# Kernel tuning notes

Hardware: AMD Instinct MI355X
Metric: run time of the kernel (lower is better)

## Reference

```python
import jax, jax.numpy as jnp
import numpy as np
from jax import lax

N, M, T, IN, H, DEPTH = 64, 10, 160, 40, 256, 3
B = N * M
EPS = 1e-8


def setup_inputs() -> dict:
    key = jax.random.key(0)
    ks = jax.random.split(key, 20)
    s = 1.0 / np.sqrt(H)  # torch LSTM init scale
    inp = {
        "sequences": jax.random.normal(ks[0], (B, T, IN), jnp.float32),
        "len_sequences": jax.random.randint(ks[1], (B,), 80, T + 1, jnp.int32),
        "w_sim": jnp.float32(0.5),
        "b_sim": jnp.float32(0.5),
    }
    in_sizes = [IN, H, H]
    for l in range(DEPTH):
        k = 2 + 4 * l
        inp[f"Wih{l}"] = jax.random.uniform(ks[k], (4 * H, in_sizes[l]), jnp.float32, -s, s)
        inp[f"Whh{l}"] = jax.random.uniform(ks[k + 1], (4 * H, H), jnp.float32, -s, s)
        inp[f"bih{l}"] = jax.random.uniform(ks[k + 2], (4 * H,), jnp.float32, -s, s)
        inp[f"bhh{l}"] = jax.random.uniform(ks[k + 3], (4 * H,), jnp.float32, -s, s)
    return inp


def _lstm_layer(x_tbf, mask_tb, Wih, Whh, bih, bhh):
    """x_tbf: [T,B,F] time-major. mask_tb: [T,B] valid-step mask.
    Returns (h_seq [T,B,H], c_last [B,H]) where c_last is the cell state at
    the last valid timestep of each sequence (packed-sequence semantics)."""
    b = x_tbf.shape[1]
    h0 = jnp.zeros((b, H), x_tbf.dtype)
    c0 = jnp.zeros((b, H), x_tbf.dtype)

    def step(carry, xm):
        h, c = carry
        xt, mt = xm
        g = xt @ Wih.T + bih + h @ Whh.T + bhh  # [B,4H]
        i, f, gg, o = jnp.split(g, 4, axis=1)
        cn = jax.nn.sigmoid(f) * c + jax.nn.sigmoid(i) * jnp.tanh(gg)
        hn = jax.nn.sigmoid(o) * jnp.tanh(cn)
        m = mt[:, None]
        h2 = jnp.where(m, hn, h)
        c2 = jnp.where(m, cn, c)
        return (h2, c2), h2

    (hT, cT), h_seq = lax.scan(step, (h0, c0), (x_tbf, mask_tb))
    return h_seq, cT


def reference(sequences, len_sequences, Wih0, Whh0, bih0, bhh0,
              Wih1, Whh1, bih1, bhh1, Wih2, Whh2, bih2, bhh2,
              w_sim, b_sim):
    lens = len_sequences.astype(jnp.int32)
    x = jnp.transpose(sequences, (1, 0, 2))  # [T,B,IN]
    mask = jnp.arange(T)[:, None] < lens[None, :]  # [T,B]

    layers = [(Wih0, Whh0, bih0, bhh0), (Wih1, Whh1, bih1, bhh1), (Wih2, Whh2, bih2, bhh2)]
    c_last = None
    for (Wih, Whh, bih, bhh) in layers:
        x, c_last = _lstm_layer(x, mask, Wih, Whh, bih, bhh)
    E = c_last  # [B,H] final-layer cell state per utterance (original order)

    # L2-normalize embeddings (F.normalize, p=2, dim=1)
    E = E / jnp.maximum(jnp.linalg.norm(E, axis=1, keepdims=True), 1e-12)

    Er = E.reshape(N, M, H)
    C = Er.mean(axis=1)  # [N,H] speaker centroids
    # exclusive centroids exactly as source: (M*c_j + E_i)/(M-1)
    Cm = ((M * C[:, None, :] + Er) / (M - 1)).reshape(B, H)

    En = E / jnp.maximum(jnp.linalg.norm(E, axis=1, keepdims=True), EPS)
    Cn = C / jnp.maximum(jnp.linalg.norm(C, axis=1, keepdims=True), EPS)
    Cmn = Cm / jnp.maximum(jnp.linalg.norm(Cm, axis=1, keepdims=True), EPS)

    S = (En @ Cn.T) * w_sim + b_sim  # [B,N]: cos(E_i, c_j)*w + b

    # diagonal block: row i, col i//M uses exclusive centroid
    d = jnp.sum(En * Cmn, axis=1)  # [B]
    rows = jnp.arange(B)
    cols = jnp.repeat(jnp.arange(N), M)
    S = S.at[rows, cols].set(d * w_sim + b_sim)
    return S


if __name__ == "__main__":
    out = reference(**setup_inputs())
    print(out.shape, out.dtype)
```

## Files before the change

kernel.cpp:

```cpp
#include <hip/hip_runtime.h>
#include <cstdint>
#include <cstddef>

typedef __attribute__((ext_vector_type(8))) short short8;
typedef __attribute__((ext_vector_type(4))) float f32x4;
typedef __attribute__((ext_vector_type(4))) unsigned short us4;

#define N_SPK 64
#define M_UTT 10
#define T_SEQ 160
#define IN_F  40
#define H_DIM 256
#define B_TOT 640
#define G4    1024
#define FSTR  64

__device__ __forceinline__ unsigned short f2bf(float f) {
  unsigned int u = __float_as_uint(f);
  u += 0x7FFFu + ((u >> 16) & 1u);
  return (unsigned short)(u >> 16);
}
__device__ __forceinline__ float b2f(unsigned short u) {
  return __uint_as_float(((unsigned int)u) << 16);
}
__device__ __forceinline__ float sigm(float x) {
  return 1.f / (1.f + __expf(-x));
}
__device__ __forceinline__ float tanh_fast(float x) {
  return 1.f - 2.f / (1.f + __expf(2.f * x));
}
__device__ __forceinline__ unsigned long long ato_ld(const unsigned long long* p) {
  return __hip_atomic_load(p, __ATOMIC_RELAXED, __HIP_MEMORY_SCOPE_AGENT);
}
__device__ __forceinline__ void ato_st(unsigned long long* p, unsigned long long v) {
  __hip_atomic_store(p, v, __ATOMIC_RELAXED, __HIP_MEMORY_SCOPE_AGENT);
}
__device__ __forceinline__ int flg_ld(const int* p) {
  return __hip_atomic_load(p, __ATOMIC_RELAXED, __HIP_MEMORY_SCOPE_AGENT);
}
__device__ __forceinline__ void flg_st(int* p, int v) {
  __hip_atomic_store(p, v, __ATOMIC_RELAXED, __HIP_MEMORY_SCOPE_AGENT);
}

__global__ void pack_w_kernel(const float* __restrict__ W, short* __restrict__ out,
                              int Kin, int Ktiles) {
  int idx = blockIdx.x * 256 + threadIdx.x;
  int total = 64 * Ktiles * 64;
  if (idx >= total) return;
  int lane = idx & 63;
  int rest = idx >> 6;
  int ks   = rest % Ktiles;
  int tile = rest / Ktiles;
  int n  = tile * 16 + (lane & 15);
  int k0 = ks * 32 + (lane >> 4) * 8;
  short8 v;
#pragma unroll
  for (int j = 0; j < 8; ++j) {
    int k = k0 + j;
    float f = (k < Kin) ? W[(size_t)n * Kin + k] : 0.f;
    v[j] = (short)f2bf(f);
  }
  *(short8*)&out[(size_t)idx * 8] = v;
}

__global__ void bias_sum_kernel(const float* __restrict__ a, const float* __restrict__ b,
                                float* __restrict__ o) {
  int i = blockIdx.x * 256 + threadIdx.x;
  if (i < G4) o[i] = a[i] + b[i];
}

__global__ __launch_bounds__(256, 2)
void gate_gemm0(const float* __restrict__ seq, const short* __restrict__ Wp,
                const float* __restrict__ bias, unsigned short* __restrict__ G) {
  const int btile = blockIdx.x % 40;
  const int rest  = blockIdx.x / 40;
  const int tg    = rest & 3;
  const int chunk = rest >> 2;
  const int tid = threadIdx.x, lane = tid & 63, wave = tid >> 6;
  const int nl = lane & 15, mq = lane >> 4;

  for (int mg = 0; mg < 4; ++mg) {
    const int t0 = chunk * 16 + mg * 4;
    f32x4 acc[4][4];
#pragma unroll
    for (int q = 0; q < 4; ++q) {
      int tile = tg * 16 + wave + 4 * q;
      float bv = bias[tile * 16 + nl];
#pragma unroll
      for (int mm = 0; mm < 4; ++mm) acc[mm][q] = (f32x4){bv, bv, bv, bv};
    }
    for (int kt = 0; kt < 2; ++kt) {
      short8 a[4];
      const int m = btile * 16 + nl;
      const int k0 = kt * 32 + mq * 8;
#pragma unroll
      for (int mm = 0; mm < 4; ++mm) {
#pragma unroll
        for (int j = 0; j < 8; ++j) {
          int k = k0 + j;
          float f = (k < IN_F) ? seq[((size_t)m * T_SEQ + (t0 + mm)) * IN_F + k] : 0.f;
          a[mm][j] = (short)f2bf(f);
        }
      }
#pragma unroll
      for (int q = 0; q < 4; ++q) {
        int tile = tg * 16 + wave + 4 * q;
        short8 b = *(const short8*)&Wp[(((size_t)tile * 2 + kt) * 64 + lane) * 8];
#pragma unroll
        for (int mm = 0; mm < 4; ++mm)
          acc[mm][q] = __builtin_amdgcn_mfma_f32_16x16x32_bf16(a[mm], b, acc[mm][q], 0, 0, 0);
      }
    }
#pragma unroll
    for (int mm = 0; mm < 4; ++mm)
#pragma unroll
      for (int q = 0; q < 4; ++q) {
        int tile = tg * 16 + wave + 4 * q;
        us4 o;
#pragma unroll
        for (int r = 0; r < 4; ++r) o[r] = f2bf(acc[mm][q][r]);
        *(us4*)&G[(((size_t)(t0 + mm) * 40 + btile) * 64 + tile) * 256 + lane * 4] = o;
      }
  }
}

template<int L>
__device__ __forceinline__ void rec_stage(
    int S, int hb,
    const short* __restrict__ Whhp, const short* __restrict__ Wihp,
    const unsigned short* __restrict__ G0, const float* __restrict__ biasl,
    unsigned long long* __restrict__ hxch, int* __restrict__ flags,
    const int* __restrict__ lens, float* __restrict__ c_state,
    unsigned short* h_sh, unsigned short* x_sh,
    float* bias_sh, short* wih_lds, int* len_sh)
{
  const int tid = threadIdx.x, lane = tid & 63, wave = tid >> 6;
  const int mq = lane >> 4, nl = lane & 15;
  const int lc = wave * 16 + nl;
  const int colown = hb * 64 + lc;
  unsigned long long* x64 = (unsigned long long*)x_sh;

  short8 wregH[4][8];
#pragma unroll
  for (int g = 0; g < 4; ++g) {
    const int tile = g * 16 + hb * 4 + wave;
#pragma unroll
    for (int kt = 0; kt < 8; ++kt)
      wregH[g][kt] = *(const short8*)&Whhp[(((size_t)tile * 8 + kt) * 64 + lane) * 8];
  }
  short8 wregI[4][4];
  if (L >= 1) {
#pragma unroll
    for (int g = 0; g < 4; ++g) {
      const int tile = g * 16 + hb * 4 + wave;
#pragma unroll
      for (int kt = 0; kt < 4; ++kt)
        wregI[g][kt] = *(const short8*)&Wihp[(((size_t)tile * 8 + kt) * 64 + lane) * 8];
    }
    for (int i = tid; i < 4096; i += 256) {
      int tl = i >> 6, ln = i & 63;
      int lt = tl >> 2, kt4 = tl & 3;
      int gt = (lt >> 2) * 16 + hb * 4 + (lt & 3);
      *(short8*)&wih_lds[(lt * 4 + kt4) * 512 + ln * 8] =
          *(const short8*)&Wihp[(((size_t)gt * 8 + 4 + kt4) * 64 + ln) * 8];
    }
    for (int i = tid; i < 1024; i += 256) bias_sh[i] = biasl[i];
  }
  for (int i = tid; i < 64 * 264; i += 256) h_sh[i] = 0;
  if (tid < 64) len_sh[tid] = lens[S * 64 + tid];

  float creg[16];
#pragma unroll
  for (int i = 0; i < 16; ++i) creg[i] = 0.f;

  if (L == 0) {
    us4 tmp[16];
#pragma unroll
    for (int m = 0; m < 4; ++m)
#pragma unroll
      for (int g = 0; g < 4; ++g) {
        const int tile = g * 16 + hb * 4 + wave;
        tmp[m * 4 + g] = *(const us4*)&G0[(((size_t)0 * 40 + S * 4 + m) * 64 + tile) * 256 + lane * 4];
      }
#pragma unroll
    for (int u = 0; u < 16; ++u)
      x64[u * 256 + tid] = *(unsigned long long*)&tmp[u];
  }
  __syncthreads();

  const int fself = L * 40 + S * 4 + hb;

  unsigned long long xr[16];
  if (L >= 1) {
    if (tid < 4)
      while (flg_ld(&flags[((L - 1) * 40 + S * 4 + tid) * FSTR]) < 1) {}
    __syncthreads();
    const unsigned long long* xb0 =
        hxch + ((size_t)((0 * 3 + (L - 1)) * 10 + S)) * 4096;
#pragma unroll
    for (int u = 0; u < 16; ++u) xr[u] = ato_ld(&xb0[u * 256 + tid]);
  }

  for (int t = 0; t < T_SEQ; ++t) {
    const int par = t & 3;

    if (L < 2 && tid < 4)
      while (flg_ld(&flags[((L + 1) * 40 + S * 4 + tid) * FSTR]) < t - 3) {}

    if (L >= 1) {
#pragma unroll
      for (int u = 0; u < 16; ++u) {
        int j = u * 256 + tid, pp = j >> 10, jj = j & 1023;
        *(unsigned long long*)&x_sh[(jj >> 4) * 264 + pp * 64 + (jj & 15) * 4] = xr[u];
      }
      __syncthreads();
    }
    f32x4 acc[4][4];
    if (L == 0) {
#pragma unroll
      for (int m = 0; m < 4; ++m)
#pragma unroll
        for (int g = 0; g < 4; ++g) {
          unsigned long long v = x64[(m * 4 + g) * 256 + tid];
          us4 gv = *(us4*)&v;
#pragma unroll
          for (int r = 0; r < 4; ++r) acc[m][g][r] = b2f(gv[r]);
        }
    } else {
#pragma unroll
      for (int g = 0; g < 4; ++g) {
        const int tile = g * 16 + hb * 4 + wave;
        float bv = bias_sh[tile * 16 + nl];
#pragma unroll
        for (int m = 0; m < 4; ++m) acc[m][g] = (f32x4){bv, bv, bv, bv};
      }
    }
#pragma unroll
    for (int kt = 0; kt < 8; ++kt) {
      short8 a[4];
#pragma unroll
      for (int m = 0; m < 4; ++m)
        a[m] = *(const short8*)&h_sh[(m * 16 + nl) * 264 + kt * 32 + mq * 8];
#pragma unroll
      for (int m = 0; m < 4; ++m)
#pragma unroll
        for (int g = 0; g < 4; ++g)
          acc[m][g] = __builtin_amdgcn_mfma_f32_16x16x32_bf16(a[m], wregH[g][kt], acc[m][g], 0, 0, 0);
    }
    if (L >= 1) {
#pragma unroll
      for (int kt = 0; kt < 8; ++kt) {
        short8 a[4];
#pragma unroll
        for (int m = 0; m < 4; ++m)
          a[m] = *(const short8*)&x_sh[(m * 16 + nl) * 264 + kt * 32 + mq * 8];
#pragma unroll
        for (int g = 0; g < 4; ++g) {
          short8 b = (kt < 4) ? wregI[g][kt]
                              : *(const short8*)&wih_lds[((g * 4 + wave) * 4 + (kt - 4)) * 512 + lane * 8];
#pragma unroll
          for (int m = 0; m < 4; ++m)
            acc[m][g] = __builtin_amdgcn_mfma_f32_16x16x32_bf16(a[m], b, acc[m][g], 0, 0, 0);
        }
      }
    }
    unsigned short hv[16];
#pragma unroll
    for (int m = 0; m < 4; ++m)
#pragma unroll
      for (int r = 0; r < 4; ++r) {
        const int row = m * 16 + mq * 4 + r;
        float c_old = creg[m * 4 + r];
        float cn = sigm(acc[m][1][r]) * c_old + sigm(acc[m][0][r]) * tanh_fast(acc[m][2][r]);
        float hn = sigm(acc[m][3][r]) * tanh_fast(cn);
        bool upd = t < len_sh[row];
        if (upd) creg[m * 4 + r] = cn;
        hv[m * 4 + r] = upd ? f2bf(hn) : h_sh[row * 264 + colown];
      }
    __syncthreads();
#pragma unroll
    for (int m = 0; m < 4; ++m)
#pragma unroll
      for (int r = 0; r < 4; ++r)
        h_sh[(m * 16 + mq * 4 + r) * 264 + colown] = hv[m * 4 + r];
    __syncthreads();
    unsigned long long* myslab =
        hxch + ((size_t)((par * 3 + L) * 10 + S) * 4 + hb) * 1024;
    for (int j = tid; j < 1024; j += 256) {
      int sample = j >> 4, l4 = j & 15;
      unsigned long long v =
          *(const unsigned long long*)&h_sh[sample * 264 + hb * 64 + l4 * 4];
      ato_st(&myslab[j], v);
    }
    __syncthreads();
    if (tid == 0) flg_st(&flags[fself * FSTR], t + 1);
    if (L == 0) {
      int tn = (t + 1 < T_SEQ) ? t + 1 : t;
      us4 tmp[16];
#pragma unroll
      for (int m = 0; m < 4; ++m)
#pragma unroll
        for (int g = 0; g < 4; ++g) {
          const int tile = g * 16 + hb * 4 + wave;
          tmp[m * 4 + g] = *(const us4*)&G0[(((size_t)tn * 40 + S * 4 + m) * 64 + tile) * 256 + lane * 4];
        }
#pragma unroll
      for (int u = 0; u < 16; ++u)
        x64[u * 256 + tid] = *(unsigned long long*)&tmp[u];
    }
    if (t + 1 < T_SEQ) {
      if (tid < 3) {
        int p = tid + (tid >= hb ? 1 : 0);
        while (flg_ld(&flags[(L * 40 + S * 4 + p) * FSTR]) < t + 1) {}
      }
      if (L >= 1 && tid >= 64 && tid < 68)
        while (flg_ld(&flags[((L - 1) * 40 + S * 4 + (tid - 64)) * FSTR]) < t + 2) {}
      __syncthreads();
      if (L >= 1) {
        const unsigned long long* xb =
            hxch + ((size_t)((((t + 1) & 3) * 3 + (L - 1)) * 10 + S)) * 4096;
#pragma unroll
        for (int u = 0; u < 16; ++u) xr[u] = ato_ld(&xb[u * 256 + tid]);
      }
      {
        unsigned long long pr[12];
#pragma unroll
        for (int u = 0; u < 12; ++u) {
          int j = u * 256 + tid;
          int pp = j >> 10, jj = j & 1023;
          int p = pp + (pp >= hb ? 1 : 0);
          pr[u] = ato_ld(&hxch[((size_t)((par * 3 + L) * 10 + S) * 4 + p) * 1024 + jj]);
        }
#pragma unroll
        for (int u = 0; u < 12; ++u) {
          int j = u * 256 + tid;
          int pp = j >> 10, jj = j & 1023;
          int p = pp + (pp >= hb ? 1 : 0);
          *(unsigned long long*)&h_sh[(jj >> 4) * 264 + p * 64 + (jj & 15) * 4] = pr[u];
        }
      }
      __syncthreads();
    }
  }
  if (L == 2) {
#pragma unroll
    for (int m = 0; m < 4; ++m)
#pragma unroll
      for (int r = 0; r < 4; ++r) {
        const int row = m * 16 + mq * 4 + r;
        c_state[((size_t)S * 64 + row) * 256 + colown] = creg[m * 4 + r];
      }
  }
}

__global__ __launch_bounds__(256, 1)
void fused_lstm(const short* __restrict__ Whhp_all, const short* __restrict__ Wih1p,
                const short* __restrict__ Wih2p, const float* __restrict__ biasc,
                const unsigned short* __restrict__ G0, const int* __restrict__ lens,
                unsigned long long* __restrict__ hxch, int* __restrict__ flags,
                float* __restrict__ c_state)
{
  __shared__ unsigned short h_sh[64 * 264];
  __shared__ unsigned short x_sh[64 * 264];
  __shared__ float bias_sh[1024];
  __shared__ short wih_lds[16 * 4 * 512];
  __shared__ int len_sh[64];

  const int bid  = blockIdx.x;
  const int xcd  = bid & 7;
  const int j    = bid >> 3;
  const int g    = (j >> 2) * 8 + xcd;
  if (g >= 30) return;
  const int L  = g / 10;
  const int S  = g % 10;
  const int hb = j & 3;

  if (L == 0)
    rec_stage<0>(S, hb, Whhp_all,          nullptr, G0, nullptr,
                 hxch, flags, lens, c_state, h_sh, x_sh, bias_sh, wih_lds, len_sh);
  else if (L == 1)
    rec_stage<1>(S, hb, Whhp_all + 262144, Wih1p, G0, biasc + G4,
                 hxch, flags, lens, c_state, h_sh, x_sh, bias_sh, wih_lds, len_sh);
  else
    rec_stage<2>(S, hb, Whhp_all + 524288, Wih2p, G0, biasc + 2 * G4,
                 hxch, flags, lens, c_state, h_sh, x_sh, bias_sh, wih_lds, len_sh);
}

__global__ void k_norm(const float* __restrict__ E, float* __restrict__ E1,
                       float* __restrict__ En) {
  int row  = blockIdx.x * 4 + (threadIdx.x >> 6);
  int lane = threadIdx.x & 63;
  const float* e = E + (size_t)row * H_DIM;
  float v[4]; float ss = 0.f;
#pragma unroll
  for (int j = 0; j < 4; ++j) { v[j] = e[lane + 64 * j]; ss += v[j] * v[j]; }
#pragma unroll
  for (int m = 32; m >= 1; m >>= 1) ss += __shfl_xor(ss, m, 64);
  float nrm  = sqrtf(ss);
  float inv1 = 1.f / fmaxf(nrm, 1e-12f);
  float inv2 = 1.f / fmaxf(nrm * inv1, 1e-8f);
#pragma unroll
  for (int j = 0; j < 4; ++j) {
    float e1 = v[j] * inv1;
    E1[(size_t)row * H_DIM + lane + 64 * j] = e1;
    En[(size_t)row * H_DIM + lane + 64 * j] = e1 * inv2;
  }
}

__global__ void k_cent(const float* __restrict__ E1, float* __restrict__ C,
                       float* __restrict__ CnT) {
  int n = blockIdx.x;
  int lane = threadIdx.x;
  float v[4]; float ss = 0.f;
#pragma unroll
  for (int j = 0; j < 4; ++j) {
    int col = lane + 64 * j;
    float s = 0.f;
    for (int m = 0; m < M_UTT; ++m) s += E1[((size_t)n * M_UTT + m) * H_DIM + col];
    v[j] = s / (float)M_UTT;
    ss += v[j] * v[j];
  }
#pragma unroll
  for (int m = 32; m >= 1; m >>= 1) ss += __shfl_xor(ss, m, 64);
  float inv = 1.f / fmaxf(sqrtf(ss), 1e-8f);
#pragma unroll
  for (int j = 0; j < 4; ++j) {
    int col = lane + 64 * j;
    C[(size_t)n * H_DIM + col]  = v[j];
    CnT[(size_t)col * N_SPK + n] = v[j] * inv;
  }
}

__global__ void k_cm(const float* __restrict__ E1, const float* __restrict__ C,
                     float* __restrict__ Cmn) {
  int b    = blockIdx.x * 4 + (threadIdx.x >> 6);
  int lane = threadIdx.x & 63;
  int spk  = b / M_UTT;
  float v[4]; float ss = 0.f;
#pragma unroll
  for (int j = 0; j < 4; ++j) {
    int col = lane + 64 * j;
    v[j] = ((float)M_UTT * C[(size_t)spk * H_DIM + col] + E1[(size_t)b * H_DIM + col])
           / (float)(M_UTT - 1);
    ss += v[j] * v[j];
  }
#pragma unroll
  for (int m = 32; m >= 1; m >>= 1) ss += __shfl_xor(ss, m, 64);
  float inv = 1.f / fmaxf(sqrtf(ss), 1e-8f);
#pragma unroll
  for (int j = 0; j < 4; ++j)
    Cmn[(size_t)b * H_DIM + lane + 64 * j] = v[j] * inv;
}

__global__ void k_sim(const float* __restrict__ En, const float* __restrict__ CnT,
                      const float* __restrict__ Cmn, const float* __restrict__ w_sim,
                      const float* __restrict__ b_sim, float* __restrict__ S) {
  int b = blockIdx.x;
  int n = threadIdx.x;
  int diag = b / M_UTT;
  float w = w_sim[0], bb = b_sim[0];
  float s = 0.f;
  for (int k = 0; k < H_DIM; ++k) {
    float en = En[(size_t)b * H_DIM + k];
    float c  = (n == diag) ? Cmn[(size_t)b * H_DIM + k] : CnT[(size_t)k * N_SPK + n];
    s += en * c;
  }
  S[(size_t)b * N_SPK + n] = s * w + bb;
}

#define O_WHH   0ull
#define O_WIH0  1572864ull
#define O_WIH1  1703936ull
#define O_WIH2  2228224ull
#define O_BIAS  2752512ull
#define O_CST   2764800ull
#define O_E1    3420160ull
#define O_EN    4075520ull
#define O_C     4730880ull
#define O_CNT   4796416ull
#define O_CMN   4861952ull
#define O_FLG   5517312ull
#define O_HXCH  5548032ull
#define O_G0    9480192ull

extern "C" void kernel_launch(void* const* d_in, const int* in_sizes, int n_in,
                              void* d_out, int out_size, void* d_ws, size_t ws_size,
                              hipStream_t stream) {
  const float* seq   = (const float*)d_in[0];
  const int*   lens  = (const int*)d_in[1];
  const float* w_sim = (const float*)d_in[2];
  const float* b_sim = (const float*)d_in[3];
  const float* Wih[3] = {(const float*)d_in[4],  (const float*)d_in[8],  (const float*)d_in[12]};
  const float* Whh[3] = {(const float*)d_in[5],  (const float*)d_in[9],  (const float*)d_in[13]};
  const float* bih[3] = {(const float*)d_in[6],  (const float*)d_in[10], (const float*)d_in[14]};
  const float* bhh[3] = {(const float*)d_in[7],  (const float*)d_in[11], (const float*)d_in[15]};

  char* ws = (char*)d_ws;
  short* Whhp_all = (short*)(ws + O_WHH);
  short* Wihp[3] = {(short*)(ws + O_WIH0), (short*)(ws + O_WIH1), (short*)(ws + O_WIH2)};
  float* biasc = (float*)(ws + O_BIAS);
  float* c_state = (float*)(ws + O_CST);
  float* E1  = (float*)(ws + O_E1);
  float* En  = (float*)(ws + O_EN);
  float* C   = (float*)(ws + O_C);
  float* CnT = (float*)(ws + O_CNT);
  float* Cmn = (float*)(ws + O_CMN);
  int* flags = (int*)(ws + O_FLG);
  unsigned long long* hxch = (unsigned long long*)(ws + O_HXCH);
  unsigned short* G0 = (unsigned short*)(ws + O_G0);
  float* S = (float*)d_out;

  pack_w_kernel<<<32, 256, 0, stream>>>(Wih[0], Wihp[0], IN_F, 2);
  pack_w_kernel<<<128, 256, 0, stream>>>(Whh[0], Whhp_all, H_DIM, 8);
  pack_w_kernel<<<128, 256, 0, stream>>>(Whh[1], Whhp_all + 262144, H_DIM, 8);
  pack_w_kernel<<<128, 256, 0, stream>>>(Whh[2], Whhp_all + 524288, H_DIM, 8);
  pack_w_kernel<<<128, 256, 0, stream>>>(Wih[1], Wihp[1], H_DIM, 8);
  pack_w_kernel<<<128, 256, 0, stream>>>(Wih[2], Wihp[2], H_DIM, 8);
  for (int l = 0; l < 3; ++l)
    bias_sum_kernel<<<4, 256, 0, stream>>>(bih[l], bhh[l], biasc + l * G4);

  gate_gemm0<<<1600, 256, 0, stream>>>(seq, Wihp[0], biasc, G0);

  hipMemsetAsync(ws + O_FLG, 0, 30720, stream);
  fused_lstm<<<128, 256, 0, stream>>>(Whhp_all, Wihp[1], Wihp[2], biasc, G0, lens,
                                      hxch, flags, c_state);

  k_norm<<<160, 256, 0, stream>>>(c_state, E1, En);
  k_cent<<<N_SPK, 64, 0, stream>>>(E1, C, CnT);
  k_cm<<<160, 256, 0, stream>>>(E1, C, Cmn);
  k_sim<<<B_TOT, 64, 0, stream>>>(En, CnT, Cmn, w_sim, b_sim, S);
}
```

Before: 1.560 ms.

## Split recurrent LSTM block across 8 waves, halving per-wave batch rows

Doubles the fused LSTM block to 512 threads: each group of four waves handles half of the 64 batch rows, so each wave issues half as many MFMAs per timestep and keeps fewer accumulators. Register pressure is relieved by keeping 7 of 8 Whh k-tiles in registers and staging the last one in LDS. The previous-layer input is now written straight into LDS instead of going through a register array. The goal is to shorten the serial per-timestep critical path, at the cost of duplicated weight registers across the two wave halves, more LDS traffic and more waves joining each barrier.

```diff
diff --git a/kernel.cpp b/kernel.cpp
--- a/kernel.cpp
+++ b/kernel.cpp
@@ -132,65 +132,74 @@
     unsigned long long* __restrict__ hxch, int* __restrict__ flags,
     const int* __restrict__ lens, float* __restrict__ c_state,
     unsigned short* h_sh, unsigned short* x_sh,
-    float* bias_sh, short* wih_lds, int* len_sh)
+    float* bias_sh, short* wih_lds, short* whh_lds, int* len_sh)
 {
-  const int tid = threadIdx.x, lane = tid & 63, wave = tid >> 6;
+  const int tid = threadIdx.x;
+  const int lane = tid & 63;
+  const int w    = tid >> 6;
+  const int wr   = w & 3;
+  const int mh   = w >> 2;
   const int mq = lane >> 4, nl = lane & 15;
-  const int lc = wave * 16 + nl;
-  const int colown = hb * 64 + lc;
+  const int colown = hb * 64 + wr * 16 + nl;
   unsigned long long* x64 = (unsigned long long*)x_sh;
 
-  short8 wregH[4][8];
+  short8 wregH[4][7];
 #pragma unroll
   for (int g = 0; g < 4; ++g) {
-    const int tile = g * 16 + hb * 4 + wave;
-#pragma unroll
-    for (int kt = 0; kt < 8; ++kt)
+    const int tile = g * 16 + hb * 4 + wr;
+#pragma unroll
+    for (int kt = 0; kt < 7; ++kt)
       wregH[g][kt] = *(const short8*)&Whhp[(((size_t)tile * 8 + kt) * 64 + lane) * 8];
+  }
+  for (int i = tid; i < 1024; i += 512) {
+    int tl = i >> 6, ln = i & 63;
+    int gt = (tl >> 2) * 16 + hb * 4 + (tl & 3);
+    *(short8*)&whh_lds[tl * 512 + ln * 8] =
+        *(const short8*)&Whhp[(((size_t)gt * 8 + 7) * 64 + ln) * 8];
   }
   short8 wregI[4][4];
   if (L >= 1) {
 #pragma unroll
     for (int g = 0; g < 4; ++g) {
-      const int tile = g * 16 + hb * 4 + wave;
+      const int tile = g * 16 + hb * 4 + wr;
 #pragma unroll
       for (int kt = 0; kt < 4; ++kt)
         wregI[g][kt] = *(const short8*)&Wihp[(((size_t)tile * 8 + kt) * 64 + lane) * 8];
     }
-    for (int i = tid; i < 4096; i += 256) {
+    for (int i = tid; i < 4096; i += 512) {
       int tl = i >> 6, ln = i & 63;
       int lt = tl >> 2, kt4 = tl & 3;
       int gt = (lt >> 2) * 16 + hb * 4 + (lt & 3);
       *(short8*)&wih_lds[(lt * 4 + kt4) * 512 + ln * 8] =
           *(const short8*)&Wihp[(((size_t)gt * 8 + 4 + kt4) * 64 + ln) * 8];
     }
-    for (int i = tid; i < 1024; i += 256) bias_sh[i] = biasl[i];
-  }
-  for (int i = tid; i < 64 * 264; i += 256) h_sh[i] = 0;
+    for (int i = tid; i < 1024; i += 512) bias_sh[i] = biasl[i];
+  }
+  for (int i = tid; i < 64 * 264; i += 512) h_sh[i] = 0;
   if (tid < 64) len_sh[tid] = lens[S * 64 + tid];
 
-  float creg[16];
-#pragma unroll
-  for (int i = 0; i < 16; ++i) creg[i] = 0.f;
+  float creg[8];
+#pragma unroll
+  for (int i = 0; i < 8; ++i) creg[i] = 0.f;
 
   if (L == 0) {
-    us4 tmp[16];
-#pragma unroll
-    for (int m = 0; m < 4; ++m)
+    us4 tmp[8];
+#pragma unroll
+    for (int mi = 0; mi < 2; ++mi)
 #pragma unroll
       for (int g = 0; g < 4; ++g) {
-        const int tile = g * 16 + hb * 4 + wave;
-        tmp[m * 4 + g] = *(const us4*)&G0[(((size_t)0 * 40 + S * 4 + m) * 64 + tile) * 256 + lane * 4];
-      }
-#pragma unroll
-    for (int u = 0; u < 16; ++u)
-      x64[u * 256 + tid] = *(unsigned long long*)&tmp[u];
+        const int m = mh * 2 + mi;
+        const int tile = g * 16 + hb * 4 + wr;
+        tmp[mi * 4 + g] = *(const us4*)&G0[(((size_t)0 * 40 + S * 4 + m) * 64 + tile) * 256 + lane * 4];
+      }
+#pragma unroll
+    for (int u = 0; u < 8; ++u)
+      x64[u * 512 + tid] = *(unsigned long long*)&tmp[u];
   }
   __syncthreads();
 
   const int fself = L * 40 + S * 4 + hb;
 
-  unsigned long long xr[16];
   if (L >= 1) {
     if (tid < 4)
       while (flg_ld(&flags[((L - 1) * 40 + S * 4 + tid) * FSTR]) < 1) {}
@@ -198,7 +207,12 @@
     const unsigned long long* xb0 =
         hxch + ((size_t)((0 * 3 + (L - 1)) * 10 + S)) * 4096;
 #pragma unroll
-    for (int u = 0; u < 16; ++u) xr[u] = ato_ld(&xb0[u * 256 + tid]);
+    for (int u = 0; u < 8; ++u) {
+      int j = u * 512 + tid, pp = j >> 10, jj = j & 1023;
+      unsigned long long v = ato_ld(&xb0[j]);
+      *(unsigned long long*)&x_sh[(jj >> 4) * 264 + pp * 64 + (jj & 15) * 4] = v;
+    }
+    __syncthreads();
   }
 
   for (int t = 0; t < T_SEQ; ++t) {
@@ -207,86 +221,81 @@
     if (L < 2 && tid < 4)
       while (flg_ld(&flags[((L + 1) * 40 + S * 4 + tid) * FSTR]) < t - 3) {}
 
+    f32x4 acc[2][4];
+    if (L == 0) {
+#pragma unroll
+      for (int mi = 0; mi < 2; ++mi)
+#pragma unroll
+        for (int g = 0; g < 4; ++g) {
+          unsigned long long v = x64[(mi * 4 + g) * 512 + tid];
+          us4 gv = *(us4*)&v;
+#pragma unroll
+          for (int r = 0; r < 4; ++r) acc[mi][g][r] = b2f(gv[r]);
+        }
+    } else {
+#pragma unroll
+      for (int g = 0; g < 4; ++g) {
+        const int tile = g * 16 + hb * 4 + wr;
+        float bv = bias_sh[tile * 16 + nl];
+#pragma unroll
+        for (int mi = 0; mi < 2; ++mi) acc[mi][g] = (f32x4){bv, bv, bv, bv};
+      }
+    }
+#pragma unroll
+    for (int kt = 0; kt < 8; ++kt) {
+      short8 a[2];
+#pragma unroll
+      for (int mi = 0; mi < 2; ++mi)
+        a[mi] = *(const short8*)&h_sh[((mh * 2 + mi) * 16 + nl) * 264 + kt * 32 + mq * 8];
+#pragma unroll
+      for (int g = 0; g < 4; ++g) {
+        short8 b = (kt < 7) ? wregH[g][kt]
+                            : *(const short8*)&whh_lds[(g * 4 + wr) * 512 + lane * 8];
+#pragma unroll
+        for (int mi = 0; mi < 2; ++mi)
+          acc[mi][g] = __builtin_amdgcn_mfma_f32_16x16x32_bf16(a[mi], b, acc[mi][g], 0, 0, 0);
+      }
+    }
     if (L >= 1) {
 #pragma unroll
-      for (int u = 0; u < 16; ++u) {
-        int j = u * 256 + tid, pp = j >> 10, jj = j & 1023;
-        *(unsigned long long*)&x_sh[(jj >> 4) * 264 + pp * 64 + (jj & 15) * 4] = xr[u];
-      }
-      __syncthreads();
-    }
-    f32x4 acc[4][4];
-    if (L == 0) {
-#pragma unroll
-      for (int m = 0; m < 4; ++m)
-#pragma unroll
-        for (int g = 0; g < 4; ++g) {
-          unsigned long long v = x64[(m * 4 + g) * 256 + tid];
-          us4 gv = *(us4*)&v;
-#pragma unroll
-          for (int r = 0; r < 4; ++r) acc[m][g][r] = b2f(gv[r]);
-        }
-    } else {
-#pragma unroll
-      for (int g = 0; g < 4; ++g) {
-        const int tile = g * 16 + hb * 4 + wave;
-        float bv = bias_sh[tile * 16 + nl];
-#pragma unroll
-        for (int m = 0; m < 4; ++m) acc[m][g] = (f32x4){bv, bv, bv, bv};
-      }
-    }
-#pragma unroll
-    for (int kt = 0; kt < 8; ++kt) {
-      short8 a[4];
-#pragma unroll
-      for (int m = 0; m < 4; ++m)
-        a[m] = *(const short8*)&h_sh[(m * 16 + nl) * 264 + kt * 32 + mq * 8];
-#pragma unroll
-      for (int m = 0; m < 4; ++m)
-#pragma unroll
-        for (int g = 0; g < 4; ++g)
-          acc[m][g] = __builtin_amdgcn_mfma_f32_16x16x32_bf16(a[m], wregH[g][kt], acc[m][g], 0, 0, 0);
-    }
-    if (L >= 1) {
-#pragma unroll
       for (int kt = 0; kt < 8; ++kt) {
-        short8 a[4];
-#pragma unroll
-        for (int m = 0; m < 4; ++m)
-          a[m] = *(const short8*)&x_sh[(m * 16 + nl) * 264 + kt * 32 + mq * 8];
+        short8 a[2];
+#pragma unroll
+        for (int mi = 0; mi < 2; ++mi)
+          a[mi] = *(const short8*)&x_sh[((mh * 2 + mi) * 16 + nl) * 264 + kt * 32 + mq * 8];
 #pragma unroll
         for (int g = 0; g < 4; ++g) {
           short8 b = (kt < 4) ? wregI[g][kt]
-                              : *(const short8*)&wih_lds[((g * 4 + wave) * 4 + (kt - 4)) * 512 + lane * 8];
-#pragma unroll
-          for (int m = 0; m < 4; ++m)
-            acc[m][g] = __builtin_amdgcn_mfma_f32_16x16x32_bf16(a[m], b, acc[m][g], 0, 0, 0);
-        }
-      }
-    }
-    unsigned short hv[16];
-#pragma unroll
-    for (int m = 0; m < 4; ++m)
+                              : *(const short8*)&wih_lds[((g * 4 + wr) * 4 + (kt - 4)) * 512 + lane * 8];
+#pragma unroll
+          for (int mi = 0; mi < 2; ++mi)
+            acc[mi][g] = __builtin_amdgcn_mfma_f32_16x16x32_bf16(a[mi], b, acc[mi][g], 0, 0, 0);
+        }
+      }
+    }
+    unsigned short hv[8];
+#pragma unroll
+    for (int mi = 0; mi < 2; ++mi)
 #pragma unroll
       for (int r = 0; r < 4; ++r) {
-        const int row = m * 16 + mq * 4 + r;
-        float c_old = creg[m * 4 + r];
-        float cn = sigm(acc[m][1][r]) * c_old + sigm(acc[m][0][r]) * tanh_fast(acc[m][2][r]);
-        float hn = sigm(acc[m][3][r]) * tanh_fast(cn);
+        const int row = (mh * 2 + mi) * 16 + mq * 4 + r;
+        float c_old = creg[mi * 4 + r];
+        float cn = sigm(acc[mi][1][r]) * c_old + sigm(acc[mi][0][r]) * tanh_fast(acc[mi][2][r]);
+        float hn = sigm(acc[mi][3][r]) * tanh_fast(cn);
         bool upd = t < len_sh[row];
-        if (upd) creg[m * 4 + r] = cn;
-        hv[m * 4 + r] = upd ? f2bf(hn) : h_sh[row * 264 + colown];
+        if (upd) creg[mi * 4 + r] = cn;
+        hv[mi * 4 + r] = upd ? f2bf(hn) : h_sh[row * 264 + colown];
       }
     __syncthreads();
 #pragma unroll
-    for (int m = 0; m < 4; ++m)
+    for (int mi = 0; mi < 2; ++mi)
 #pragma unroll
       for (int r = 0; r < 4; ++r)
-        h_sh[(m * 16 + mq * 4 + r) * 264 + colown] = hv[m * 4 + r];
+        h_sh[((mh * 2 + mi) * 16 + mq * 4 + r) * 264 + colown] = hv[mi * 4 + r];
     __syncthreads();
     unsigned long long* myslab =
         hxch + ((size_t)((par * 3 + L) * 10 + S) * 4 + hb) * 1024;
-    for (int j = tid; j < 1024; j += 256) {
+    for (int j = tid; j < 1024; j += 512) {
       int sample = j >> 4, l4 = j & 15;
       unsigned long long v =
           *(const unsigned long long*)&h_sh[sample * 264 + hb * 64 + l4 * 4];
@@ -296,17 +305,18 @@
     if (tid == 0) flg_st(&flags[fself * FSTR], t + 1);
     if (L == 0) {
       int tn = (t + 1 < T_SEQ) ? t + 1 : t;
-      us4 tmp[16];
-#pragma unroll
-      for (int m = 0; m < 4; ++m)
+      us4 tmp[8];
+#pragma unroll
+      for (int mi = 0; mi < 2; ++mi)
 #pragma unroll
         for (int g = 0; g < 4; ++g) {
-          const int tile = g * 16 + hb * 4 + wave;
-          tmp[m * 4 + g] = *(const us4*)&G0[(((size_t)tn * 40 + S * 4 + m) * 64 + tile) * 256 + lane * 4];
-        }
-#pragma unroll
-      for (int u = 0; u < 16; ++u)
-        x64[u * 256 + tid] = *(unsigned long long*)&tmp[u];
+          const int m = mh * 2 + mi;
+          const int tile = g * 16 + hb * 4 + wr;
+          tmp[mi * 4 + g] = *(const us4*)&G0[(((size_t)tn * 40 + S * 4 + m) * 64 + tile) * 256 + lane * 4];
+        }
+#pragma unroll
+      for (int u = 0; u < 8; ++u)
+        x64[u * 512 + tid] = *(unsigned long long*)&tmp[u];
     }
     if (t + 1 < T_SEQ) {
       if (tid < 3) {
@@ -320,20 +330,24 @@
         const unsigned long long* xb =
             hxch + ((size_t)((((t + 1) & 3) * 3 + (L - 1)) * 10 + S)) * 4096;
 #pragma unroll
-        for (int u = 0; u < 16; ++u) xr[u] = ato_ld(&xb[u * 256 + tid]);
+        for (int u = 0; u < 8; ++u) {
+          int j = u * 512 + tid, pp = j >> 10, jj = j & 1023;
+          unsigned long long v = ato_ld(&xb[j]);
+          *(unsigned long long*)&x_sh[(jj >> 4) * 264 + pp * 64 + (jj & 15) * 4] = v;
+        }
       }
       {
-        unsigned long long pr[12];
-#pragma unroll
-        for (int u = 0; u < 12; ++u) {
-          int j = u * 256 + tid;
+        unsigned long long pr[6];
+#pragma unroll
+        for (int u = 0; u < 6; ++u) {
+          int j = u * 512 + tid;
           int pp = j >> 10, jj = j & 1023;
           int p = pp + (pp >= hb ? 1 : 0);
           pr[u] = ato_ld(&hxch[((size_t)((par * 3 + L) * 10 + S) * 4 + p) * 1024 + jj]);
         }
 #pragma unroll
-        for (int u = 0; u < 12; ++u) {
-          int j = u * 256 + tid;
+        for (int u = 0; u < 6; ++u) {
+          int j = u * 512 + tid;
           int pp = j >> 10, jj = j & 1023;
           int p = pp + (pp >= hb ? 1 : 0);
           *(unsigned long long*)&h_sh[(jj >> 4) * 264 + p * 64 + (jj & 15) * 4] = pr[u];
@@ -344,16 +358,16 @@
   }
   if (L == 2) {
 #pragma unroll
-    for (int m = 0; m < 4; ++m)
+    for (int mi = 0; mi < 2; ++mi)
 #pragma unroll
       for (int r = 0; r < 4; ++r) {
-        const int row = m * 16 + mq * 4 + r;
-        c_state[((size_t)S * 64 + row) * 256 + colown] = creg[m * 4 + r];
-      }
-  }
-}
-
-__global__ __launch_bounds__(256, 1)
+        const int row = (mh * 2 + mi) * 16 + mq * 4 + r;
+        c_state[((size_t)S * 64 + row) * 256 + colown] = creg[mi * 4 + r];
+      }
+  }
+}
+
+__global__ __launch_bounds__(512, 2)
 void fused_lstm(const short* __restrict__ Whhp_all, const short* __restrict__ Wih1p,
                 const short* __restrict__ Wih2p, const float* __restrict__ biasc,
                 const unsigned short* __restrict__ G0, const int* __restrict__ lens,
@@ -364,6 +378,7 @@
   __shared__ unsigned short x_sh[64 * 264];
   __shared__ float bias_sh[1024];
   __shared__ short wih_lds[16 * 4 * 512];
+  __shared__ short whh_lds[16 * 512];
   __shared__ int len_sh[64];
 
   const int bid  = blockIdx.x;
@@ -377,13 +392,13 @@
 
   if (L == 0)
     rec_stage<0>(S, hb, Whhp_all,          nullptr, G0, nullptr,
-                 hxch, flags, lens, c_state, h_sh, x_sh, bias_sh, wih_lds, len_sh);
+                 hxch, flags, lens, c_state, h_sh, x_sh, bias_sh, wih_lds, whh_lds, len_sh);
   else if (L == 1)
     rec_stage<1>(S, hb, Whhp_all + 262144, Wih1p, G0, biasc + G4,
-                 hxch, flags, lens, c_state, h_sh, x_sh, bias_sh, wih_lds, len_sh);
+                 hxch, flags, lens, c_state, h_sh, x_sh, bias_sh, wih_lds, whh_lds, len_sh);
   else
     rec_stage<2>(S, hb, Whhp_all + 524288, Wih2p, G0, biasc + 2 * G4,
-                 hxch, flags, lens, c_state, h_sh, x_sh, bias_sh, wih_lds, len_sh);
+                 hxch, flags, lens, c_state, h_sh, x_sh, bias_sh, wih_lds, whh_lds, len_sh);
 }
 
 __global__ void k_norm(const float* __restrict__ E, float* __restrict__ E1,
@@ -521,8 +536,8 @@
 
   gate_gemm0<<<1600, 256, 0, stream>>>(seq, Wihp[0], biasc, G0);
 
-  hipMemsetAsync(ws + O_FLG, 0, 30720, stream);
-  fused_lstm<<<128, 256, 0, stream>>>(Whhp_all, Wihp[1], Wihp[2], biasc, G0, lens,
+  (void)hipMemsetAsync(ws + O_FLG, 0, 30720, stream);
+  fused_lstm<<<128, 512, 0, stream>>>(Whhp_all, Wihp[1], Wihp[2], biasc, G0, lens,
                                       hxch, flags, c_state);
 
   k_norm<<<160, 256, 0, stream>>>(c_state, E1, En);
```

Result: slower. 1.840 ms (+18.0%).

## Overlap peer hidden-state exchange with local-slice recurrent MFMAs and input projection

Applied to the files above, without the earlier changes.

The recurrent K loop is rotated so each block first multiplies the K slices it produced itself (already in LDS), then the input projection, and only then writes the peer blocks' h values into LDS and finishes the remaining slices. The cross-block exchange loads now land in registers at the end of the previous step and are stored into LDS later, which hides global-load latency behind MFMA work. One __syncthreads is replaced by a lighter LDS-only barrier. This shortens the critical path of each serial timestep, at the cost of extra register pressure from keeping pr[] live across the step.

```diff
diff --git a/kernel.cpp b/kernel.cpp
--- a/kernel.cpp
+++ b/kernel.cpp
@@ -41,6 +41,12 @@
 __device__ __forceinline__ void flg_st(int* p, int v) {
   __hip_atomic_store(p, v, __ATOMIC_RELAXED, __HIP_MEMORY_SCOPE_AGENT);
 }
+
+#define LDS_BARRIER() do {                                      \
+  asm volatile("s_waitcnt lgkmcnt(0)" ::: "memory");            \
+  __builtin_amdgcn_s_barrier();                                 \
+  asm volatile("" ::: "memory");                                \
+} while (0)
 
 __global__ void pack_w_kernel(const float* __restrict__ W, short* __restrict__ out,
                               int Kin, int Ktiles) {
@@ -145,8 +151,10 @@
   for (int g = 0; g < 4; ++g) {
     const int tile = g * 16 + hb * 4 + wave;
 #pragma unroll
-    for (int kt = 0; kt < 8; ++kt)
-      wregH[g][kt] = *(const short8*)&Whhp[(((size_t)tile * 8 + kt) * 64 + lane) * 8];
+    for (int s = 0; s < 8; ++s) {
+      const int ktp = (2 * hb + s) & 7;
+      wregH[g][s] = *(const short8*)&Whhp[(((size_t)tile * 8 + ktp) * 64 + lane) * 8];
+    }
   }
   short8 wregI[4][4];
   if (L >= 1) {
@@ -200,6 +208,7 @@
 #pragma unroll
     for (int u = 0; u < 16; ++u) xr[u] = ato_ld(&xb0[u * 256 + tid]);
   }
+  unsigned long long pr[12];
 
   for (int t = 0; t < T_SEQ; ++t) {
     const int par = t & 3;
@@ -207,47 +216,46 @@
     if (L < 2 && tid < 4)
       while (flg_ld(&flags[((L + 1) * 40 + S * 4 + tid) * FSTR]) < t - 3) {}
 
+    f32x4 acc[4][4];
+    if (L == 0) {
+#pragma unroll
+      for (int m = 0; m < 4; ++m)
+#pragma unroll
+        for (int g = 0; g < 4; ++g) {
+          unsigned long long v = x64[(m * 4 + g) * 256 + tid];
+          us4 gv = *(us4*)&v;
+#pragma unroll
+          for (int r = 0; r < 4; ++r) acc[m][g][r] = b2f(gv[r]);
+        }
+    } else {
+#pragma unroll
+      for (int g = 0; g < 4; ++g) {
+        const int tile = g * 16 + hb * 4 + wave;
+        float bv = bias_sh[tile * 16 + nl];
+#pragma unroll
+        for (int m = 0; m < 4; ++m) acc[m][g] = (f32x4){bv, bv, bv, bv};
+      }
+    }
+#pragma unroll
+    for (int s = 0; s < 2; ++s) {
+      const int ktp = (2 * hb + s) & 7;
+      short8 a[4];
+#pragma unroll
+      for (int m = 0; m < 4; ++m)
+        a[m] = *(const short8*)&h_sh[(m * 16 + nl) * 264 + ktp * 32 + mq * 8];
+#pragma unroll
+      for (int m = 0; m < 4; ++m)
+#pragma unroll
+        for (int g = 0; g < 4; ++g)
+          acc[m][g] = __builtin_amdgcn_mfma_f32_16x16x32_bf16(a[m], wregH[g][s], acc[m][g], 0, 0, 0);
+    }
     if (L >= 1) {
 #pragma unroll
       for (int u = 0; u < 16; ++u) {
         int j = u * 256 + tid, pp = j >> 10, jj = j & 1023;
         *(unsigned long long*)&x_sh[(jj >> 4) * 264 + pp * 64 + (jj & 15) * 4] = xr[u];
       }
-      __syncthreads();
-    }
-    f32x4 acc[4][4];
-    if (L == 0) {
-#pragma unroll
-      for (int m = 0; m < 4; ++m)
-#pragma unroll
-        for (int g = 0; g < 4; ++g) {
-          unsigned long long v = x64[(m * 4 + g) * 256 + tid];
-          us4 gv = *(us4*)&v;
-#pragma unroll
-          for (int r = 0; r < 4; ++r) acc[m][g][r] = b2f(gv[r]);
-        }
-    } else {
-#pragma unroll
-      for (int g = 0; g < 4; ++g) {
-        const int tile = g * 16 + hb * 4 + wave;
-        float bv = bias_sh[tile * 16 + nl];
-#pragma unroll
-        for (int m = 0; m < 4; ++m) acc[m][g] = (f32x4){bv, bv, bv, bv};
-      }
-    }
-#pragma unroll
-    for (int kt = 0; kt < 8; ++kt) {
-      short8 a[4];
-#pragma unroll
-      for (int m = 0; m < 4; ++m)
-        a[m] = *(const short8*)&h_sh[(m * 16 + nl) * 264 + kt * 32 + mq * 8];
-#pragma unroll
-      for (int m = 0; m < 4; ++m)
-#pragma unroll
-        for (int g = 0; g < 4; ++g)
-          acc[m][g] = __builtin_amdgcn_mfma_f32_16x16x32_bf16(a[m], wregH[g][kt], acc[m][g], 0, 0, 0);
-    }
-    if (L >= 1) {
+      LDS_BARRIER();
 #pragma unroll
       for (int kt = 0; kt < 8; ++kt) {
         short8 a[4];
@@ -263,6 +271,29 @@
             acc[m][g] = __builtin_amdgcn_mfma_f32_16x16x32_bf16(a[m], b, acc[m][g], 0, 0, 0);
         }
       }
+    }
+    if (t > 0) {
+#pragma unroll
+      for (int u = 0; u < 12; ++u) {
+        int j = u * 256 + tid;
+        int pp = j >> 10, jj = j & 1023;
+        int p = pp + (pp >= hb ? 1 : 0);
+        *(unsigned long long*)&h_sh[(jj >> 4) * 264 + p * 64 + (jj & 15) * 4] = pr[u];
+      }
+    }
+    __syncthreads();
+#pragma unroll
+    for (int s = 2; s < 8; ++s) {
+      const int ktp = (2 * hb + s) & 7;
+      short8 a[4];
+#pragma unroll
+      for (int m = 0; m < 4; ++m)
+        a[m] = *(const short8*)&h_sh[(m * 16 + nl) * 264 + ktp * 32 + mq * 8];
+#pragma unroll
+      for (int m = 0; m < 4; ++m)
+#pragma unroll
+        for (int g = 0; g < 4; ++g)
+          acc[m][g] = __builtin_amdgcn_mfma_f32_16x16x32_bf16(a[m], wregH[g][s], acc[m][g], 0, 0, 0);
     }
     unsigned short hv[16];
 #pragma unroll
@@ -322,24 +353,13 @@
 #pragma unroll
         for (int u = 0; u < 16; ++u) xr[u] = ato_ld(&xb[u * 256 + tid]);
       }
-      {
-        unsigned long long pr[12];
-#pragma unroll
-        for (int u = 0; u < 12; ++u) {
-          int j = u * 256 + tid;
-          int pp = j >> 10, jj = j & 1023;
-          int p = pp + (pp >= hb ? 1 : 0);
-          pr[u] = ato_ld(&hxch[((size_t)((par * 3 + L) * 10 + S) * 4 + p) * 1024 + jj]);
-        }
-#pragma unroll
-        for (int u = 0; u < 12; ++u) {
-          int j = u * 256 + tid;
-          int pp = j >> 10, jj = j & 1023;
-          int p = pp + (pp >= hb ? 1 : 0);
-          *(unsigned long long*)&h_sh[(jj >> 4) * 264 + p * 64 + (jj & 15) * 4] = pr[u];
-        }
-      }
-      __syncthreads();
+#pragma unroll
+      for (int u = 0; u < 12; ++u) {
+        int j = u * 256 + tid;
+        int pp = j >> 10, jj = j & 1023;
+        int p = pp + (pp >= hb ? 1 : 0);
+        pr[u] = ato_ld(&hxch[((size_t)((par * 3 + L) * 10 + S) * 4 + p) * 1024 + jj]);
+      }
     }
   }
   if (L == 2) {
@@ -521,7 +541,7 @@
 
   gate_gemm0<<<1600, 256, 0, stream>>>(seq, Wihp[0], biasc, G0);
 
-  hipMemsetAsync(ws + O_FLG, 0, 30720, stream);
+  (void)hipMemsetAsync(ws + O_FLG, 0, 30720, stream);
   fused_lstm<<<128, 256, 0, stream>>>(Whhp_all, Wihp[1], Wihp[2], biasc, G0, lens,
                                       hxch, flags, c_state);
 
```

Result: slower. 1.663 ms (+6.6%).
